# Kernel optimization log

Measured on AMD Instinct MI355X. Metric: run time of the kernel, lower is better.

## Reference

```python
import jax, jax.numpy as jnp
import numpy as np

N_NODES = 50000
N_EDGES = 600000
IN_DIM = 128
HID_DIM = 512
OUT_DIM = 2


def setup_inputs() -> dict:
    key = jax.random.key(0)
    ks = jax.random.split(key, 8)
    x = jax.random.normal(ks[0], (N_NODES, IN_DIM), dtype=jnp.float32)
    edge_index = jax.random.randint(ks[1], (2, N_EDGES), 0, N_NODES, dtype=jnp.int32)
    s1 = 1.0 / np.sqrt(IN_DIM)
    s2 = 1.0 / np.sqrt(HID_DIM)
    # SAGEConv params: lin_l (applied to mean-aggregated neighbors, has bias),
    # lin_r (applied to root node features, no bias)
    W1l = jax.random.uniform(ks[2], (IN_DIM, HID_DIM), jnp.float32, -s1, s1)
    b1 = jax.random.uniform(ks[3], (HID_DIM,), jnp.float32, -s1, s1)
    W1r = jax.random.uniform(ks[4], (IN_DIM, HID_DIM), jnp.float32, -s1, s1)
    W2l = jax.random.uniform(ks[5], (HID_DIM, OUT_DIM), jnp.float32, -s2, s2)
    b2 = jax.random.uniform(ks[6], (OUT_DIM,), jnp.float32, -s2, s2)
    W2r = jax.random.uniform(ks[7], (HID_DIM, OUT_DIM), jnp.float32, -s2, s2)
    return {"x": x, "W1l": W1l, "b1": b1, "W1r": W1r,
            "W2l": W2l, "b2": b2, "W2r": W2r, "edge_index": edge_index}


def _sage_conv(x, edge_index, Wl, b, Wr):
    src, dst = edge_index[0], edge_index[1]
    msgs = x[src]                                             # [E, d]
    agg = jax.ops.segment_sum(msgs, dst, num_segments=x.shape[0])  # [N, d]
    deg = jax.ops.segment_sum(jnp.ones_like(dst, dtype=x.dtype), dst,
                              num_segments=x.shape[0])
    agg = agg / jnp.maximum(deg, 1.0)[:, None]                # mean aggregation
    return agg @ Wl + b + x @ Wr


def reference(x, W1l, b1, W1r, W2l, b2, W2r, edge_index):
    h = _sage_conv(x, edge_index, W1l, b1, W1r)
    h = jax.nn.relu(h)
    # dropout inactive (eval mode / force_dropout=False)
    out = _sage_conv(h, edge_index, W2l, b2, W2r)
    return jax.nn.log_softmax(out, axis=1)
```

## Files before the change

### kernel.cpp

```cpp
#include <hip/hip_runtime.h>
#include <math.h>
#include <stdint.h>

#define N_NODES 50000
#define N_EDGES 600000
#define IN_DIM 128
#define HID_DIM 512
#define M_PAD 50048
#define SCAN_NB 196
#define NPAD 50048

#define NB_C 128
#define CE4_C 1172
#define HALF_N 25024
#define H2W 12512
#define HIST_NB 256

#define CASTX_NB5 3125
#define CASTW_NB5 272

typedef __bf16 bf16;
typedef __bf16 bf16x2 __attribute__((ext_vector_type(2)));
typedef __bf16 bf16x4 __attribute__((ext_vector_type(4)));
typedef __bf16 bf16x8 __attribute__((ext_vector_type(8)));
typedef float f32x4 __attribute__((ext_vector_type(4)));

#define GLDS(gp, lp) __builtin_amdgcn_global_load_lds( \
    (const __attribute__((address_space(1))) uint32_t*)(gp), \
    (__attribute__((address_space(3))) uint32_t*)(lp), 16, 0, 0)


__global__ __launch_bounds__(512) void histcast_kernel(
    const int* __restrict__ dst, uint32_t* __restrict__ Hg32,
    const float* __restrict__ x, bf16* __restrict__ xb,
    const float* __restrict__ W1l, const float* __restrict__ W1r,
    const float* __restrict__ W2l, const float* __restrict__ W2r,
    bf16* __restrict__ Wt, bf16* __restrict__ W2bt) {
    __shared__ uint32_t h2[H2W];
    int b = blockIdx.x, t = threadIdx.x;
    if (b < HIST_NB) {
        for (int j = t; j < H2W; j += 512) h2[j] = 0;
        __syncthreads();
        int c = b >> 1, h = b & 1;
        int base = h * HALF_N;
        int e40 = c * CE4_C;
        int e4end = min(e40 + CE4_C, N_EDGES / 4);
        for (int e4 = e40 + t; e4 < e4end; e4 += 512) {
            int4 d = ((const int4*)dst)[e4];
            unsigned v0 = (unsigned)(d.x - base);
            unsigned v1 = (unsigned)(d.y - base);
            unsigned v2 = (unsigned)(d.z - base);
            unsigned v3 = (unsigned)(d.w - base);
            if (v0 < HALF_N) atomicAdd(&h2[v0 >> 1], 1u << ((v0 & 1) << 4));
            if (v1 < HALF_N) atomicAdd(&h2[v1 >> 1], 1u << ((v1 & 1) << 4));
            if (v2 < HALF_N) atomicAdd(&h2[v2 >> 1], 1u << ((v2 & 1) << 4));
            if (v3 < HALF_N) atomicAdd(&h2[v3 >> 1], 1u << ((v3 & 1) << 4));
        }
        __syncthreads();
        uint32_t* outp = Hg32 + (size_t)c * (NPAD / 2) + (size_t)h * H2W;
        for (int j = t; j < H2W; j += 512) outp[j] = h2[j];
    } else if (b < HIST_NB + CASTX_NB5) {
        int i = (b - HIST_NB) * 512 + t;
        float4 v = ((const float4*)x)[i];
        bf16x4 o = {(bf16)v.x, (bf16)v.y, (bf16)v.z, (bf16)v.w};
        *(bf16x4*)(xb + (size_t)i * 4) = o;
    } else {
        int idx = (b - HIST_NB - CASTX_NB5) * 512 + t;
        if (idx < 512 * 256) {
            int n = idx >> 8;
            int k = idx & 255;
            float v = (k < IN_DIM) ? W1l[(size_t)k * HID_DIM + n]
                                   : W1r[(size_t)(k - IN_DIM) * HID_DIM + n];
            Wt[idx] = (bf16)v;
        } else {
            int j = idx - 512 * 256;
            int n = j >> 9;
            int k = j & 511;
            float v = 0.f;
            if (n == 0) v = W2l[k * 2 + 0];
            else if (n == 1) v = W2l[k * 2 + 1];
            else if (n == 2) v = W2r[k * 2 + 0];
            else if (n == 3) v = W2r[k * 2 + 1];
            W2bt[j] = (bf16)v;
        }
    }
}


__global__ __launch_bounds__(256) void scancols_kernel(
    const uint16_t* __restrict__ Hg, int* __restrict__ deg,
    uint16_t* __restrict__ PB, int* __restrict__ bsum) {
    int t = threadIdx.x;
    int n = blockIdx.x * 256 + t;
    int running = 0;
    if (n < NPAD) {
#pragma unroll 8
        for (int c = 0; c < NB_C; ++c) {
            int v = Hg[(size_t)c * NPAD + n];
            PB[(size_t)c * NPAD + n] = (uint16_t)running;
            running += v;
        }
        deg[n] = running;
    }
    int v = (n < N_NODES) ? running : 0;
#pragma unroll
    for (int m = 1; m < 64; m <<= 1) v += __shfl_xor(v, m);
    __shared__ int ws_[4];
    int w = t >> 6, l = t & 63;
    if (l == 0) ws_[w] = v;
    __syncthreads();
    if (t == 0) bsum[blockIdx.x] = ws_[0] + ws_[1] + ws_[2] + ws_[3];
}

__global__ __launch_bounds__(256) void scan3_kernel(const int* __restrict__ deg,
                                                    const int* __restrict__ bsum,
                                                    int* __restrict__ offsets) {
    int t = threadIdx.x;
    int blk = blockIdx.x;
    int i = blk * 256 + t;
    int l = t & 63, w = t >> 6;
    int v = (i < N_NODES) ? deg[i] : 0;
    int inc = v;
#pragma unroll
    for (int off = 1; off < 64; off <<= 1) {
        int y = __shfl_up(inc, off);
        if (l >= off) inc += y;
    }
    __shared__ int wsum[4];
    __shared__ int lookback;
    if (l == 63) wsum[w] = inc;
    __syncthreads();
    if (t < 64) {
        int s = 0;
        for (int u = t; u < blk; u += 64) s += bsum[u];
#pragma unroll
        for (int m = 1; m < 64; m <<= 1) s += __shfl_xor(s, m);
        if (t == 0) lookback = s;
    }
    __syncthreads();
    int add = lookback;
    for (int u = 0; u < w; ++u) add += wsum[u];
    int ex = add + inc - v;
    if (i < N_NODES) offsets[i] = ex;
    if (blk == 0 && t == 0) offsets[N_NODES] = N_EDGES;
}


__global__ __launch_bounds__(512) void fill_kernel(
    const int* __restrict__ src, const int* __restrict__ dst,
    const int* __restrict__ offsets, const uint16_t* __restrict__ PB,
    int* __restrict__ csr_src) {
    __shared__ uint32_t h2[H2W];
    int b = blockIdx.x, t = threadIdx.x;
    for (int j = t; j < H2W; j += 512) h2[j] = 0;
    __syncthreads();
    int c = b >> 1, h = b & 1;
    int base = h * HALF_N;
    const uint16_t* pb = PB + (size_t)c * NPAD;
    int e40 = c * CE4_C;
    int e4end = min(e40 + CE4_C, N_EDGES / 4);
    for (int e4 = e40 + t; e4 < e4end; e4 += 512) {
        int4 d = ((const int4*)dst)[e4];
        int4 s = ((const int4*)src)[e4];
        unsigned v0 = (unsigned)(d.x - base);
        unsigned v1 = (unsigned)(d.y - base);
        unsigned v2 = (unsigned)(d.z - base);
        unsigned v3 = (unsigned)(d.w - base);
        if (v0 < HALF_N) {
            int sh = (v0 & 1) << 4;
            uint32_t r = atomicAdd(&h2[v0 >> 1], 1u << sh);
            csr_src[offsets[d.x] + (int)pb[d.x] + (int)((r >> sh) & 0xffff)] = s.x;
        }
        if (v1 < HALF_N) {
            int sh = (v1 & 1) << 4;
            uint32_t r = atomicAdd(&h2[v1 >> 1], 1u << sh);
            csr_src[offsets[d.y] + (int)pb[d.y] + (int)((r >> sh) & 0xffff)] = s.y;
        }
        if (v2 < HALF_N) {
            int sh = (v2 & 1) << 4;
            uint32_t r = atomicAdd(&h2[v2 >> 1], 1u << sh);
            csr_src[offsets[d.z] + (int)pb[d.z] + (int)((r >> sh) & 0xffff)] = s.z;
        }
        if (v3 < HALF_N) {
            int sh = (v3 & 1) << 4;
            uint32_t r = atomicAdd(&h2[v3 >> 1], 1u << sh);
            csr_src[offsets[d.w] + (int)pb[d.w] + (int)((r >> sh) & 0xffff)] = s.w;
        }
    }
}


__global__ __launch_bounds__(256) void agg1_kernel(
    const bf16* __restrict__ xb, const int* __restrict__ offsets,
    const int* __restrict__ csr_src, bf16* __restrict__ agg1b) {
    int t = threadIdx.x;
    int w = t >> 6, l = t & 63;
    int g = l >> 4;
    int sl = l & 15;
    int n = blockIdx.x * 16 + w * 4 + g;
    int s0 = offsets[n], s1 = offsets[n + 1];
    float a[8] = {};
    int e = s0;
    for (; e + 4 <= s1; e += 4) {
        int i0 = csr_src[e + 0];
        int i1 = csr_src[e + 1];
        int i2 = csr_src[e + 2];
        int i3 = csr_src[e + 3];
        bf16x8 v0 = *(const bf16x8*)(xb + (size_t)i0 * IN_DIM + sl * 8);
        bf16x8 v1 = *(const bf16x8*)(xb + (size_t)i1 * IN_DIM + sl * 8);
        bf16x8 v2 = *(const bf16x8*)(xb + (size_t)i2 * IN_DIM + sl * 8);
        bf16x8 v3 = *(const bf16x8*)(xb + (size_t)i3 * IN_DIM + sl * 8);
#pragma unroll
        for (int u = 0; u < 8; ++u)
            a[u] += (float)v0[u] + (float)v1[u] + (float)v2[u] + (float)v3[u];
    }
    for (; e < s1; ++e) {
        int i0 = csr_src[e];
        bf16x8 v0 = *(const bf16x8*)(xb + (size_t)i0 * IN_DIM + sl * 8);
#pragma unroll
        for (int u = 0; u < 8; ++u) a[u] += (float)v0[u];
    }
    float inv = 1.0f / fmaxf((float)(s1 - s0), 1.0f);
    bf16x8 o;
#pragma unroll
    for (int u = 0; u < 8; ++u) o[u] = (bf16)(a[u] * inv);
    *(bf16x8*)(agg1b + (size_t)n * IN_DIM + sl * 8) = o;
}


__global__ __launch_bounds__(256) void gemm1_kernel(
    const bf16* __restrict__ agg1b, const bf16* __restrict__ xb,
    const bf16* __restrict__ Wt, const float* __restrict__ b1,
    const bf16* __restrict__ W2bt, float* __restrict__ zpart) {
    __shared__ __align__(16) char smem[128 * 136 * 2];
    bf16 (*As)[128][32] = (bf16(*)[128][32])smem;
    bf16 (*Bs)[128][32] = (bf16(*)[128][32])(smem + 16384);
    bf16 (*Hs)[136] = (bf16(*)[136])smem;
    int tid = threadIdx.x;
    int w = tid >> 6;
    int lane = tid & 63;
    int q = lane >> 4, rr = lane & 15;
    int cb = blockIdx.x;
    int n0 = cb * 128;
    int row0 = blockIdx.y * 128;
    int wm = (w & 1) * 64, wn = (w >> 1) * 64;
    int lr = lane >> 2;
    int lc = (lane & 3) * 8;

    auto stage = [&](int ki) {
        const bf16* Asrc;
        int kb;
        if (ki < 4) { Asrc = agg1b; kb = ki * 32; }
        else        { Asrc = xb;    kb = ki * 32 - IN_DIM; }
        int kw = ki * 32;
        int buf = ki & 1;
#pragma unroll
        for (int j = 0; j < 2; ++j) {
            int r = w * 32 + j * 16 + lr;
            GLDS(Asrc + (size_t)(row0 + r) * IN_DIM + kb + lc,
                 &As[buf][w * 32 + j * 16][0]);
            GLDS(Wt + (size_t)(n0 + r) * 256 + kw + lc,
                 &Bs[buf][w * 32 + j * 16][0]);
        }
    };

    f32x4 acc[4][4] = {};
    stage(0);
#pragma unroll
    for (int ki = 0; ki < 8; ++ki) {
        __syncthreads();
        if (ki + 1 < 8) stage(ki + 1);
        int buf = ki & 1;
        bf16x8 af[4], bfr[4];
#pragma unroll
        for (int i = 0; i < 4; ++i)
            af[i] = *(const bf16x8*)&As[buf][wm + i * 16 + rr][q * 8];
#pragma unroll
        for (int j = 0; j < 4; ++j)
            bfr[j] = *(const bf16x8*)&Bs[buf][wn + j * 16 + rr][q * 8];
#pragma unroll
        for (int i = 0; i < 4; ++i)
#pragma unroll
            for (int j = 0; j < 4; ++j)
                acc[i][j] = __builtin_amdgcn_mfma_f32_16x16x32_bf16(
                    af[i], bfr[j], acc[i][j], 0, 0, 0);
    }
    __syncthreads();
    float bias[4];
#pragma unroll
    for (int j = 0; j < 4; ++j) bias[j] = b1[n0 + wn + j * 16 + rr];
#pragma unroll
    for (int i = 0; i < 4; ++i) {
#pragma unroll
        for (int rg = 0; rg < 4; ++rg) {
            int mrow = wm + i * 16 + q * 4 + rg;
#pragma unroll
            for (int j = 0; j < 4; ++j)
                Hs[mrow][wn + j * 16 + rr] =
                    (bf16)fmaxf(acc[i][j][rg] + bias[j], 0.f);
        }
    }
    __syncthreads();
    bf16x8 wf[4];
#pragma unroll
    for (int ks = 0; ks < 4; ++ks)
        wf[ks] = *(const bf16x8*)(W2bt + (size_t)rr * 512 + n0 + ks * 32 + q * 8);
    f32x4 zacc[2] = {};
#pragma unroll
    for (int mt = 0; mt < 2; ++mt)
#pragma unroll
        for (int ks = 0; ks < 4; ++ks) {
            bf16x8 afz = *(const bf16x8*)&Hs[w * 32 + mt * 16 + rr][ks * 32 + q * 8];
            zacc[mt] = __builtin_amdgcn_mfma_f32_16x16x32_bf16(
                afz, wf[ks], zacc[mt], 0, 0, 0);
        }
    if (rr < 4) {
#pragma unroll
        for (int mt = 0; mt < 2; ++mt)
#pragma unroll
            for (int rg = 0; rg < 4; ++rg) {
                int grow = row0 + w * 32 + mt * 16 + q * 4 + rg;
                zpart[(size_t)grow * 16 + cb * 4 + rr] = zacc[mt][rg];
            }
    }
}


__global__ __launch_bounds__(256) void zsum_kernel(const float* __restrict__ zpart,
                                                   float* __restrict__ z) {
    int n = blockIdx.x * blockDim.x + threadIdx.x;
    if (n >= N_NODES) return;
    const float4* p = (const float4*)(zpart + (size_t)n * 16);
    float4 a = p[0], b = p[1], c = p[2], d = p[3];
    float4 o = {a.x + b.x + c.x + d.x, a.y + b.y + c.y + d.y,
                a.z + b.z + c.z + d.z, a.w + b.w + c.w + d.w};
    *(float4*)(z + (size_t)n * 4) = o;
}


__global__ __launch_bounds__(256) void final_kernel(
    const float* __restrict__ z, const int* __restrict__ offsets,
    const int* __restrict__ csr_src, const float* __restrict__ b2,
    float* __restrict__ out) {
    int t = threadIdx.x;
    int lane4 = t & 3;
    int n = blockIdx.x * 64 + (t >> 2);
    int s0 = 0, s1 = 0;
    if (n < N_NODES) { s0 = offsets[n]; s1 = offsets[n + 1]; }
    float a0 = 0.f, a1 = 0.f;
    for (int e = s0 + lane4; e < s1; e += 4) {
        int s = csr_src[e];
        float2 v = *(const float2*)(z + (size_t)s * 4);
        a0 += v.x;
        a1 += v.y;
    }
    a0 += __shfl_xor(a0, 1); a0 += __shfl_xor(a0, 2);
    a1 += __shfl_xor(a1, 1); a1 += __shfl_xor(a1, 2);
    if (n < N_NODES && lane4 == 0) {
        float inv = 1.0f / fmaxf((float)(s1 - s0), 1.0f);
        float2 zs = *(const float2*)(z + (size_t)n * 4 + 2);
        float o0 = a0 * inv + b2[0] + zs.x;
        float o1 = a1 * inv + b2[1] + zs.y;
        float m = fmaxf(o0, o1);
        float lse = logf(expf(o0 - m) + expf(o1 - m));
        float2 o = {o0 - m - lse, o1 - m - lse};
        *(float2*)(out + (size_t)n * 2) = o;
    }
}


extern "C" void kernel_launch(void* const* d_in, const int* in_sizes, int n_in,
                              void* d_out, int out_size, void* d_ws, size_t ws_size,
                              hipStream_t stream) {
    const float* x   = (const float*)d_in[0];
    const float* W1l = (const float*)d_in[1];
    const float* b1  = (const float*)d_in[2];
    const float* W1r = (const float*)d_in[3];
    const float* W2l = (const float*)d_in[4];
    const float* b2  = (const float*)d_in[5];
    const float* W2r = (const float*)d_in[6];
    const int* edge  = (const int*)d_in[7];
    const int* src = edge;
    const int* dst = edge + N_EDGES;
    float* out = (float*)d_out;

    char* ws = (char*)d_ws;
    size_t off = 0;
    auto alloc = [&](size_t bytes) -> void* {
        void* p = ws + off;
        off += (bytes + 255) & ~(size_t)255;
        return p;
    };
    int* deg     = (int*)alloc((size_t)NPAD * 4);
    int* offsets = (int*)alloc((size_t)(N_NODES + 1) * 4);
    int* csr_src = (int*)alloc((size_t)N_EDGES * 4);
    int* bsum    = (int*)alloc((size_t)SCAN_NB * 4);
    bf16* xb     = (bf16*)alloc((size_t)M_PAD * IN_DIM * 2);
    bf16* agg1b  = (bf16*)alloc((size_t)M_PAD * IN_DIM * 2);
    bf16* Wt     = (bf16*)alloc((size_t)HID_DIM * 256 * 2);
    bf16* W2bt   = (bf16*)alloc((size_t)16 * HID_DIM * 2);
    float* zpart = (float*)alloc((size_t)M_PAD * 16 * 4);
    float* z     = (float*)alloc((size_t)N_NODES * 4 * 4);
    uint16_t* PB = (uint16_t*)alloc((size_t)NB_C * NPAD * 2);

    uint32_t* Hg32 = (uint32_t*)agg1b;

    histcast_kernel<<<HIST_NB + CASTX_NB5 + CASTW_NB5, 512, 0, stream>>>(
        dst, Hg32, x, xb, W1l, W1r, W2l, W2r, Wt, W2bt);
    scancols_kernel<<<SCAN_NB, 256, 0, stream>>>(
        (const uint16_t*)Hg32, deg, PB, bsum);
    scan3_kernel<<<SCAN_NB, 256, 0, stream>>>(deg, bsum, offsets);
    fill_kernel<<<HIST_NB, 512, 0, stream>>>(src, dst, offsets, PB, csr_src);
    agg1_kernel<<<N_NODES / 16, 256, 0, stream>>>(xb, offsets, csr_src, agg1b);
    gemm1_kernel<<<dim3(4, M_PAD / 128), 256, 0, stream>>>(
        agg1b, xb, Wt, b1, W2bt, zpart);
    zsum_kernel<<<(N_NODES + 255) / 256, 256, 0, stream>>>(zpart, z);
    final_kernel<<<(N_NODES + 63) / 64, 256, 0, stream>>>(z, offsets, csr_src, b2, out);
}
```

Measured before the change: 172.4 us.

## Compress CSR indices to 16-bit, widen gemm1 tiles, fuse zsum via last-block counter

Stores CSR source indices as uint16, which halves index traffic in fill, agg1 and final. This is only valid because node ids stay below 65536, and the 50000-node count fits that. Gemm1 now uses 512-thread blocks covering 256 output columns, so only 2 column blocks write partial z instead of 4. The separate zsum kernel is removed: the last block to arrive for each row tile, detected with an atomic counter, sums the partials. This saves a launch and a pass over memory, at the cost of fences, atomics and a more complex gemm tile mapping.

```diff
diff --git a/kernel.cpp b/kernel.cpp
--- a/kernel.cpp
+++ b/kernel.cpp
@@ -9,6 +9,7 @@
 #define M_PAD 50048
 #define SCAN_NB 196
 #define NPAD 50048
+#define NROWB 391
 
 #define NB_C 128
 #define CE4_C 1172
@@ -35,7 +36,8 @@
     const float* __restrict__ x, bf16* __restrict__ xb,
     const float* __restrict__ W1l, const float* __restrict__ W1r,
     const float* __restrict__ W2l, const float* __restrict__ W2r,
-    bf16* __restrict__ Wt, bf16* __restrict__ W2bt) {
+    bf16* __restrict__ Wt, bf16* __restrict__ W2bt,
+    int* __restrict__ cnt) {
     __shared__ uint32_t h2[H2W];
     int b = blockIdx.x, t = threadIdx.x;
     if (b < HIST_NB) {
@@ -60,6 +62,7 @@
         uint32_t* outp = Hg32 + (size_t)c * (NPAD / 2) + (size_t)h * H2W;
         for (int j = t; j < H2W; j += 512) outp[j] = h2[j];
     } else if (b < HIST_NB + CASTX_NB5) {
+        if (b == HIST_NB && t < NROWB) cnt[t] = 0;
         int i = (b - HIST_NB) * 512 + t;
         float4 v = ((const float4*)x)[i];
         bf16x4 o = {(bf16)v.x, (bf16)v.y, (bf16)v.z, (bf16)v.w};
@@ -149,7 +152,7 @@
 __global__ __launch_bounds__(512) void fill_kernel(
     const int* __restrict__ src, const int* __restrict__ dst,
     const int* __restrict__ offsets, const uint16_t* __restrict__ PB,
-    int* __restrict__ csr_src) {
+    uint16_t* __restrict__ csr) {
     __shared__ uint32_t h2[H2W];
     int b = blockIdx.x, t = threadIdx.x;
     for (int j = t; j < H2W; j += 512) h2[j] = 0;
@@ -169,22 +172,22 @@
         if (v0 < HALF_N) {
             int sh = (v0 & 1) << 4;
             uint32_t r = atomicAdd(&h2[v0 >> 1], 1u << sh);
-            csr_src[offsets[d.x] + (int)pb[d.x] + (int)((r >> sh) & 0xffff)] = s.x;
+            csr[offsets[d.x] + (int)pb[d.x] + (int)((r >> sh) & 0xffff)] = (uint16_t)s.x;
         }
         if (v1 < HALF_N) {
             int sh = (v1 & 1) << 4;
             uint32_t r = atomicAdd(&h2[v1 >> 1], 1u << sh);
-            csr_src[offsets[d.y] + (int)pb[d.y] + (int)((r >> sh) & 0xffff)] = s.y;
+            csr[offsets[d.y] + (int)pb[d.y] + (int)((r >> sh) & 0xffff)] = (uint16_t)s.y;
         }
         if (v2 < HALF_N) {
             int sh = (v2 & 1) << 4;
             uint32_t r = atomicAdd(&h2[v2 >> 1], 1u << sh);
-            csr_src[offsets[d.z] + (int)pb[d.z] + (int)((r >> sh) & 0xffff)] = s.z;
+            csr[offsets[d.z] + (int)pb[d.z] + (int)((r >> sh) & 0xffff)] = (uint16_t)s.z;
         }
         if (v3 < HALF_N) {
             int sh = (v3 & 1) << 4;
             uint32_t r = atomicAdd(&h2[v3 >> 1], 1u << sh);
-            csr_src[offsets[d.w] + (int)pb[d.w] + (int)((r >> sh) & 0xffff)] = s.w;
+            csr[offsets[d.w] + (int)pb[d.w] + (int)((r >> sh) & 0xffff)] = (uint16_t)s.w;
         }
     }
 }
@@ -192,7 +195,7 @@
 
 __global__ __launch_bounds__(256) void agg1_kernel(
     const bf16* __restrict__ xb, const int* __restrict__ offsets,
-    const int* __restrict__ csr_src, bf16* __restrict__ agg1b) {
+    const uint16_t* __restrict__ csr, bf16* __restrict__ agg1b) {
     int t = threadIdx.x;
     int w = t >> 6, l = t & 63;
     int g = l >> 4;
@@ -202,10 +205,10 @@
     float a[8] = {};
     int e = s0;
     for (; e + 4 <= s1; e += 4) {
-        int i0 = csr_src[e + 0];
-        int i1 = csr_src[e + 1];
-        int i2 = csr_src[e + 2];
-        int i3 = csr_src[e + 3];
+        int i0 = csr[e + 0];
+        int i1 = csr[e + 1];
+        int i2 = csr[e + 2];
+        int i3 = csr[e + 3];
         bf16x8 v0 = *(const bf16x8*)(xb + (size_t)i0 * IN_DIM + sl * 8);
         bf16x8 v1 = *(const bf16x8*)(xb + (size_t)i1 * IN_DIM + sl * 8);
         bf16x8 v2 = *(const bf16x8*)(xb + (size_t)i2 * IN_DIM + sl * 8);
@@ -215,7 +218,7 @@
             a[u] += (float)v0[u] + (float)v1[u] + (float)v2[u] + (float)v3[u];
     }
     for (; e < s1; ++e) {
-        int i0 = csr_src[e];
+        int i0 = csr[e];
         bf16x8 v0 = *(const bf16x8*)(xb + (size_t)i0 * IN_DIM + sl * 8);
 #pragma unroll
         for (int u = 0; u < 8; ++u) a[u] += (float)v0[u];
@@ -228,21 +231,24 @@
 }
 
 
-__global__ __launch_bounds__(256) void gemm1_kernel(
+__global__ __launch_bounds__(512, 4) void gemm1_kernel(
     const bf16* __restrict__ agg1b, const bf16* __restrict__ xb,
     const bf16* __restrict__ Wt, const float* __restrict__ b1,
-    const bf16* __restrict__ W2bt, float* __restrict__ zpart) {
-    __shared__ __align__(16) char smem[128 * 136 * 2];
+    const bf16* __restrict__ W2bt, float* __restrict__ zpart,
+    float* __restrict__ z, int* __restrict__ cnt) {
+    __shared__ __align__(16) char smem[128 * 264 * 2];
     bf16 (*As)[128][32] = (bf16(*)[128][32])smem;
-    bf16 (*Bs)[128][32] = (bf16(*)[128][32])(smem + 16384);
-    bf16 (*Hs)[136] = (bf16(*)[136])smem;
+    bf16 (*Bs)[256][32] = (bf16(*)[256][32])(smem + 16384);
+    bf16 (*Hs)[264] = (bf16(*)[264])smem;
+    __shared__ int sh_last;
     int tid = threadIdx.x;
     int w = tid >> 6;
     int lane = tid & 63;
     int q = lane >> 4, rr = lane & 15;
     int cb = blockIdx.x;
-    int n0 = cb * 128;
-    int row0 = blockIdx.y * 128;
+    int n0 = cb * 256;
+    int by = blockIdx.y;
+    int row0 = by * 128;
     int wm = (w & 1) * 64, wn = (w >> 1) * 64;
     int lr = lane >> 2;
     int lc = (lane & 3) * 8;
@@ -254,11 +260,14 @@
         else        { Asrc = xb;    kb = ki * 32 - IN_DIM; }
         int kw = ki * 32;
         int buf = ki & 1;
+        {
+            int r = w * 16 + lr;
+            GLDS(Asrc + (size_t)(row0 + r) * IN_DIM + kb + lc,
+                 &As[buf][w * 16][0]);
+        }
 #pragma unroll
         for (int j = 0; j < 2; ++j) {
             int r = w * 32 + j * 16 + lr;
-            GLDS(Asrc + (size_t)(row0 + r) * IN_DIM + kb + lc,
-                 &As[buf][w * 32 + j * 16][0]);
             GLDS(Wt + (size_t)(n0 + r) * 256 + kw + lc,
                  &Bs[buf][w * 32 + j * 16][0]);
         }
@@ -301,46 +310,45 @@
         }
     }
     __syncthreads();
-    bf16x8 wf[4];
-#pragma unroll
-    for (int ks = 0; ks < 4; ++ks)
+    bf16x8 wf[8];
+#pragma unroll
+    for (int ks = 0; ks < 8; ++ks)
         wf[ks] = *(const bf16x8*)(W2bt + (size_t)rr * 512 + n0 + ks * 32 + q * 8);
-    f32x4 zacc[2] = {};
-#pragma unroll
-    for (int mt = 0; mt < 2; ++mt)
-#pragma unroll
-        for (int ks = 0; ks < 4; ++ks) {
-            bf16x8 afz = *(const bf16x8*)&Hs[w * 32 + mt * 16 + rr][ks * 32 + q * 8];
-            zacc[mt] = __builtin_amdgcn_mfma_f32_16x16x32_bf16(
-                afz, wf[ks], zacc[mt], 0, 0, 0);
-        }
+    f32x4 zacc = {};
+#pragma unroll
+    for (int ks = 0; ks < 8; ++ks) {
+        bf16x8 afz = *(const bf16x8*)&Hs[w * 16 + rr][ks * 32 + q * 8];
+        zacc = __builtin_amdgcn_mfma_f32_16x16x32_bf16(afz, wf[ks], zacc, 0, 0, 0);
+    }
     if (rr < 4) {
 #pragma unroll
-        for (int mt = 0; mt < 2; ++mt)
-#pragma unroll
-            for (int rg = 0; rg < 4; ++rg) {
-                int grow = row0 + w * 32 + mt * 16 + q * 4 + rg;
-                zpart[(size_t)grow * 16 + cb * 4 + rr] = zacc[mt][rg];
-            }
-    }
-}
-
-
-__global__ __launch_bounds__(256) void zsum_kernel(const float* __restrict__ zpart,
-                                                   float* __restrict__ z) {
-    int n = blockIdx.x * blockDim.x + threadIdx.x;
-    if (n >= N_NODES) return;
-    const float4* p = (const float4*)(zpart + (size_t)n * 16);
-    float4 a = p[0], b = p[1], c = p[2], d = p[3];
-    float4 o = {a.x + b.x + c.x + d.x, a.y + b.y + c.y + d.y,
-                a.z + b.z + c.z + d.z, a.w + b.w + c.w + d.w};
-    *(float4*)(z + (size_t)n * 4) = o;
+        for (int rg = 0; rg < 4; ++rg) {
+            int grow = row0 + w * 16 + q * 4 + rg;
+            __hip_atomic_store(&zpart[(size_t)grow * 8 + cb * 4 + rr], zacc[rg],
+                               __ATOMIC_RELAXED, __HIP_MEMORY_SCOPE_AGENT);
+        }
+    }
+    __threadfence();
+    __syncthreads();
+    if (tid == 0)
+        sh_last = __hip_atomic_fetch_add(&cnt[by], 1, __ATOMIC_ACQ_REL,
+                                         __HIP_MEMORY_SCOPE_AGENT);
+    __syncthreads();
+    if (sh_last == 1) {
+        int n = row0 + (tid >> 2);
+        int c = tid & 3;
+        float v0 = __hip_atomic_load(&zpart[(size_t)n * 8 + c],
+                                     __ATOMIC_RELAXED, __HIP_MEMORY_SCOPE_AGENT);
+        float v1 = __hip_atomic_load(&zpart[(size_t)n * 8 + 4 + c],
+                                     __ATOMIC_RELAXED, __HIP_MEMORY_SCOPE_AGENT);
+        z[(size_t)n * 4 + c] = v0 + v1;
+    }
 }
 
 
 __global__ __launch_bounds__(256) void final_kernel(
     const float* __restrict__ z, const int* __restrict__ offsets,
-    const int* __restrict__ csr_src, const float* __restrict__ b2,
+    const uint16_t* __restrict__ csr, const float* __restrict__ b2,
     float* __restrict__ out) {
     int t = threadIdx.x;
     int lane4 = t & 3;
@@ -349,7 +357,7 @@
     if (n < N_NODES) { s0 = offsets[n]; s1 = offsets[n + 1]; }
     float a0 = 0.f, a1 = 0.f;
     for (int e = s0 + lane4; e < s1; e += 4) {
-        int s = csr_src[e];
+        int s = csr[e];
         float2 v = *(const float2*)(z + (size_t)s * 4);
         a0 += v.x;
         a1 += v.y;
@@ -391,29 +399,29 @@
         off += (bytes + 255) & ~(size_t)255;
         return p;
     };
-    int* deg     = (int*)alloc((size_t)NPAD * 4);
-    int* offsets = (int*)alloc((size_t)(N_NODES + 1) * 4);
-    int* csr_src = (int*)alloc((size_t)N_EDGES * 4);
-    int* bsum    = (int*)alloc((size_t)SCAN_NB * 4);
-    bf16* xb     = (bf16*)alloc((size_t)M_PAD * IN_DIM * 2);
-    bf16* agg1b  = (bf16*)alloc((size_t)M_PAD * IN_DIM * 2);
-    bf16* Wt     = (bf16*)alloc((size_t)HID_DIM * 256 * 2);
-    bf16* W2bt   = (bf16*)alloc((size_t)16 * HID_DIM * 2);
-    float* zpart = (float*)alloc((size_t)M_PAD * 16 * 4);
-    float* z     = (float*)alloc((size_t)N_NODES * 4 * 4);
-    uint16_t* PB = (uint16_t*)alloc((size_t)NB_C * NPAD * 2);
+    int* deg      = (int*)alloc((size_t)NPAD * 4);
+    int* offsets  = (int*)alloc((size_t)(N_NODES + 1) * 4);
+    uint16_t* csr = (uint16_t*)alloc((size_t)N_EDGES * 2);
+    int* bsum     = (int*)alloc((size_t)SCAN_NB * 4);
+    int* cnt      = (int*)alloc((size_t)NROWB * 4);
+    bf16* xb      = (bf16*)alloc((size_t)M_PAD * IN_DIM * 2);
+    bf16* agg1b   = (bf16*)alloc((size_t)M_PAD * IN_DIM * 2);
+    bf16* Wt      = (bf16*)alloc((size_t)HID_DIM * 256 * 2);
+    bf16* W2bt    = (bf16*)alloc((size_t)16 * HID_DIM * 2);
+    float* zpart  = (float*)alloc((size_t)M_PAD * 8 * 4);
+    float* z      = (float*)alloc((size_t)M_PAD * 4 * 4);
+    uint16_t* PB  = (uint16_t*)alloc((size_t)NB_C * NPAD * 2);
 
     uint32_t* Hg32 = (uint32_t*)agg1b;
 
     histcast_kernel<<<HIST_NB + CASTX_NB5 + CASTW_NB5, 512, 0, stream>>>(
-        dst, Hg32, x, xb, W1l, W1r, W2l, W2r, Wt, W2bt);
+        dst, Hg32, x, xb, W1l, W1r, W2l, W2r, Wt, W2bt, cnt);
     scancols_kernel<<<SCAN_NB, 256, 0, stream>>>(
         (const uint16_t*)Hg32, deg, PB, bsum);
     scan3_kernel<<<SCAN_NB, 256, 0, stream>>>(deg, bsum, offsets);
-    fill_kernel<<<HIST_NB, 512, 0, stream>>>(src, dst, offsets, PB, csr_src);
-    agg1_kernel<<<N_NODES / 16, 256, 0, stream>>>(xb, offsets, csr_src, agg1b);
-    gemm1_kernel<<<dim3(4, M_PAD / 128), 256, 0, stream>>>(
-        agg1b, xb, Wt, b1, W2bt, zpart);
-    zsum_kernel<<<(N_NODES + 255) / 256, 256, 0, stream>>>(zpart, z);
-    final_kernel<<<(N_NODES + 63) / 64, 256, 0, stream>>>(z, offsets, csr_src, b2, out);
-}
+    fill_kernel<<<HIST_NB, 512, 0, stream>>>(src, dst, offsets, PB, csr);
+    agg1_kernel<<<N_NODES / 16, 256, 0, stream>>>(xb, offsets, csr, agg1b);
+    gemm1_kernel<<<dim3(2, NROWB), 512, 0, stream>>>(
+        agg1b, xb, Wt, b1, W2bt, zpart, z, cnt);
+    final_kernel<<<(N_NODES + 63) / 64, 256, 0, stream>>>(z, offsets, csr, b2, out);
+}
```

Result: slower. 263.1 us (+52.6%).
